# Optimization experiments

Measured on AMD Instinct MI355X. Metric: run time of the kernel, lower is better.

## Reference

```python
import jax, jax.numpy as jnp
import numpy as np

EPS = 1e-5


def gcn_conv(x, W, b, src, dst, ew, num_nodes):
    """GCNConv with add_self_loops=True, symmetric normalization (PyG default)."""
    # degree at destination, self-loop weight 1.0 included implicitly
    deg = jax.ops.segment_sum(ew, dst, num_segments=num_nodes) + 1.0  # [N]
    dinv = jax.lax.rsqrt(deg)                                         # deg >= 1
    norm = dinv[src] * ew * dinv[dst]                                 # [E]
    h = x @ W                                                         # [N, F]
    msg = norm[:, None] * h[src]                                      # [E, F]
    agg = jax.ops.segment_sum(msg, dst, num_segments=num_nodes)       # [N, F]
    # self-loop contribution: dinv[i] * 1 * dinv[i] = 1/deg[i]
    agg = agg + h * (1.0 / deg)[:, None]
    return agg + b


def batchnorm(h, gamma, beta):
    mean = jnp.mean(h, axis=0)
    var = jnp.mean(jnp.square(h - mean), axis=0)  # biased, training-mode stats
    return (h - mean) * jax.lax.rsqrt(var + EPS) * gamma + beta


def setup_inputs() -> dict:
    key = jax.random.key(0)
    ks = jax.random.split(key, 8)
    N, E, F = 50000, 800000, 64
    x = jax.random.normal(ks[0], (N, F), dtype=jnp.float32)
    edge_index = jax.random.randint(ks[1], (2, E), 0, N, dtype=jnp.int64)
    edge_weight = jax.random.uniform(ks[2], (E,), dtype=jnp.float32)
    s = 1.0 / np.sqrt(F)
    W1 = jax.random.uniform(ks[3], (F, F), jnp.float32, -s, s)
    b1 = jnp.zeros((F,), jnp.float32)
    W2 = jax.random.uniform(ks[4], (F, F), jnp.float32, -s, s)
    b2 = jnp.zeros((F,), jnp.float32)
    gamma1 = jnp.ones((F,), jnp.float32)
    beta1 = jnp.zeros((F,), jnp.float32)
    gamma2 = jnp.ones((F,), jnp.float32)
    beta2 = jnp.zeros((F,), jnp.float32)
    return {"x": x, "edge_index": edge_index, "edge_weight": edge_weight,
            "W1": W1, "b1": b1, "gamma1": gamma1, "beta1": beta1,
            "W2": W2, "b2": b2, "gamma2": gamma2, "beta2": beta2}


def reference(x, edge_index, edge_weight, W1, b1, gamma1, beta1, W2, b2, gamma2, beta2):
    N = x.shape[0]
    src, dst = edge_index[0], edge_index[1]
    identity = x
    out = gcn_conv(x, W1, b1, src, dst, edge_weight, N)
    out = jax.nn.relu(batchnorm(out, gamma1, beta1))
    out = gcn_conv(out, W2, b2, src, dst, edge_weight, N)
    out = batchnorm(out, gamma2, beta2)
    out = out + identity  # residual: num_input_features == hidden_dim
    return jax.nn.relu(out)
```

## Files before the change

### kernel.cpp

```cpp
#include <hip/hip_runtime.h>
#include <math.h>

#define FEAT 64
#define BN_EPS 1e-5f
#define BN_REPS 64

__device__ __forceinline__ int edge_idx(const void* p, int is64, long long i) {
    return is64 ? (int)((const long long*)p)[i] : ((const int*)p)[i];
}

__device__ __forceinline__ float4 f4fma(float a, float4 b, float4 c) {
    return make_float4(fmaf(a, b.x, c.x), fmaf(a, b.y, c.y),
                       fmaf(a, b.z, c.z), fmaf(a, b.w, c.w));
}

__device__ __forceinline__ unsigned bf16rtne(float f) {
    unsigned u = __float_as_uint(f);
    return (u + 0x7fffu + ((u >> 16) & 1u)) >> 16;
}
__device__ __forceinline__ unsigned packbf2(float a, float b) {
    return bf16rtne(a) | (bf16rtne(b) << 16);
}
__device__ __forceinline__ float4 unpackbf4(uint2 r) {
    return make_float4(__uint_as_float(r.x << 16),
                       __uint_as_float(r.x & 0xffff0000u),
                       __uint_as_float(r.y << 16),
                       __uint_as_float(r.y & 0xffff0000u));
}

__global__ __launch_bounds__(256) void init_kernel(
    const unsigned* __restrict__ w, int* __restrict__ flag,
    int* __restrict__ cnt, float* __restrict__ parts, int N) {
    int i = blockIdx.x * 256 + threadIdx.x;
    if (i < N) cnt[i] = 0;
    if (blockIdx.x < 64) parts[blockIdx.x * 256 + threadIdx.x] = 0.0f;
    if (blockIdx.x == 0 && threadIdx.x < 64) {
        unsigned long long ok = __ballot(w[2 * threadIdx.x + 1] == 0u);
        if (threadIdx.x == 0) *flag = (ok == ~0ull);
    }
}

__global__ __launch_bounds__(256) void count_seq_kernel(
    const void* __restrict__ ei, const int* __restrict__ flag,
    int* __restrict__ cnt, int* __restrict__ seq, int E) {
    int is64 = *flag;
    int T = gridDim.x * 256;
    int i = blockIdx.x * 256 + threadIdx.x;
#pragma unroll
    for (int u = 0; u < 8; ++u) {
        int e = i + u * T;
        if (e < E) {
            int dst = edge_idx(ei, is64, (long long)E + e);
            seq[e] = atomicAdd(&cnt[dst], 1);
        }
    }
}

__global__ __launch_bounds__(256) void scan1_kernel(const int* __restrict__ cnt,
                                                    int* __restrict__ excl,
                                                    int* __restrict__ bsum, int N) {
    __shared__ int tmp[256];
    int i = blockIdx.x * 256 + threadIdx.x;
    int v = (i < N) ? cnt[i] : 0;
    tmp[threadIdx.x] = v;
    __syncthreads();
    for (int off = 1; off < 256; off <<= 1) {
        int t = (threadIdx.x >= off) ? tmp[threadIdx.x - off] : 0;
        __syncthreads();
        tmp[threadIdx.x] += t;
        __syncthreads();
    }
    if (i < N) excl[i] = tmp[threadIdx.x] - v;
    if (threadIdx.x == 255) bsum[blockIdx.x] = tmp[255];
}

__global__ __launch_bounds__(256) void scan2_kernel(int* __restrict__ bsum, int nb) {
    __shared__ int tmp[256];
    int i = threadIdx.x;
    int v = (i < nb) ? bsum[i] : 0;
    tmp[i] = v;
    __syncthreads();
    for (int off = 1; off < 256; off <<= 1) {
        int t = (i >= off) ? tmp[i - off] : 0;
        __syncthreads();
        tmp[i] += t;
        __syncthreads();
    }
    if (i < nb) bsum[i] = tmp[i] - v;
}

__global__ void scan3_kernel(const int* __restrict__ excl,
                             const int* __restrict__ bsum,
                             int* __restrict__ rowptr, int N, int E) {
    int i = blockIdx.x * 256 + threadIdx.x;
    if (i < N) rowptr[i] = excl[i] + bsum[blockIdx.x];
    if (i == 0) rowptr[N] = E;
}

__global__ __launch_bounds__(256) void scatter_csr_kernel(
    const void* __restrict__ ei, const float* __restrict__ ew,
    const int* __restrict__ flag, const int* __restrict__ rowptr,
    const int* __restrict__ seq, int2* __restrict__ csr, int E) {
    int is64 = *flag;
    int T = gridDim.x * 256;
    int i = blockIdx.x * 256 + threadIdx.x;
#pragma unroll
    for (int u = 0; u < 2; ++u) {
        int e = i + u * T;
        if (e < E) {
            int src = edge_idx(ei, is64, e);
            int dst = edge_idx(ei, is64, (long long)E + e);
            int pos = rowptr[dst] + seq[e];
            csr[pos] = make_int2(src, __float_as_int(ew[e]));
        }
    }
}

__global__ __launch_bounds__(256) void deg_inv_kernel(
    const int* __restrict__ rowptr, const int2* __restrict__ csr,
    float* __restrict__ dinv, float* __restrict__ invdeg, int N) {
    int t = blockIdx.x * 256 + threadIdx.x;
    int n = t >> 3, l = t & 7;
    if (n >= N) return;
    int b = rowptr[n], e = rowptr[n + 1];
    float d = 0.0f;
    for (int k = b + l; k < e; k += 8) d += __int_as_float(csr[k].y);
    d += __shfl_xor(d, 1);
    d += __shfl_xor(d, 2);
    d += __shfl_xor(d, 4);
    if (l == 0) {
        d += 1.0f;
        dinv[n]   = rsqrtf(d);
        invdeg[n] = 1.0f / d;
    }
}

__global__ __launch_bounds__(256) void fold_kernel(int2* __restrict__ csr,
                                                   const float* __restrict__ dinv,
                                                   int E) {
    int T = gridDim.x * 256;
    int i = blockIdx.x * 256 + threadIdx.x;
#pragma unroll
    for (int u = 0; u < 2; ++u) {
        int e = i + u * T;
        if (e < E) {
            int2 v = csr[e];
            csr[e].y = __float_as_int(dinv[v.x] * __int_as_float(v.y));
        }
    }
}

__global__ __launch_bounds__(256) void gemm64_kernel(
    const float* __restrict__ in, const float* __restrict__ W,
    const float* __restrict__ scale, const float* __restrict__ shift,
    uint2* __restrict__ out_bf, int N, int affine) {
    __shared__ float4 Ws4[64][16];
    __shared__ float xs[64][65];
    __shared__ float sA[64], sS[64];
    int tid = threadIdx.x;
    const float4* W4 = (const float4*)W;
    for (int j = tid; j < 1024; j += 256) Ws4[j >> 4][j & 15] = W4[j];
    if (affine && tid < 64) { sA[tid] = scale[tid]; sS[tid] = shift[tid]; }
    __syncthreads();

    int rowBase = blockIdx.x * 64;
    for (int j = tid; j < 1024; j += 256) {
        int r = j >> 4, q = j & 15;
        int row = rowBase + r;
        float4 v = make_float4(0.f, 0.f, 0.f, 0.f);
        if (row < N) {
            v = ((const float4*)in)[(size_t)row * 16 + q];
            if (affine) {
                int c = q * 4;
                v.x = fmaxf(fmaf(v.x, sA[c + 0], sS[c + 0]), 0.f);
                v.y = fmaxf(fmaf(v.y, sA[c + 1], sS[c + 1]), 0.f);
                v.z = fmaxf(fmaf(v.z, sA[c + 2], sS[c + 2]), 0.f);
                v.w = fmaxf(fmaf(v.w, sA[c + 3], sS[c + 3]), 0.f);
            }
        }
        xs[r][q * 4 + 0] = v.x;
        xs[r][q * 4 + 1] = v.y;
        xs[r][q * 4 + 2] = v.z;
        xs[r][q * 4 + 3] = v.w;
    }
    __syncthreads();

    int q = tid & 15, rg = tid >> 4;
    int r0 = rg * 4;
    float4 a0 = make_float4(0.f, 0.f, 0.f, 0.f), a1 = a0, a2 = a0, a3 = a0;
#pragma unroll 4
    for (int k = 0; k < 64; ++k) {
        float4 wv = Ws4[k][q];
        a0 = f4fma(xs[r0 + 0][k], wv, a0);
        a1 = f4fma(xs[r0 + 1][k], wv, a1);
        a2 = f4fma(xs[r0 + 2][k], wv, a2);
        a3 = f4fma(xs[r0 + 3][k], wv, a3);
    }
    int row = rowBase + r0;
    if (row + 0 < N) out_bf[(size_t)(row + 0) * 16 + q] = make_uint2(packbf2(a0.x, a0.y), packbf2(a0.z, a0.w));
    if (row + 1 < N) out_bf[(size_t)(row + 1) * 16 + q] = make_uint2(packbf2(a1.x, a1.y), packbf2(a1.z, a1.w));
    if (row + 2 < N) out_bf[(size_t)(row + 2) * 16 + q] = make_uint2(packbf2(a2.x, a2.y), packbf2(a2.z, a2.w));
    if (row + 3 < N) out_bf[(size_t)(row + 3) * 16 + q] = make_uint2(packbf2(a3.x, a3.y), packbf2(a3.z, a3.w));
}

__global__ __launch_bounds__(256) void gather_agg_kernel(
    const uint2* __restrict__ h2, const int* __restrict__ rowptr,
    const int2* __restrict__ csr, const float* __restrict__ dinv,
    const float* __restrict__ invdeg, const float* __restrict__ bias,
    float* __restrict__ agg, float* __restrict__ parts, int N) {
    int tid = threadIdx.x;
    int wave = tid >> 6, lane = tid & 63;
    int sub = lane >> 4, sl = lane & 15;
    float4 bv = ((const float4*)bias)[sl];
    float4 bnS = make_float4(0.f, 0.f, 0.f, 0.f), bnQ = bnS;

    int n = blockIdx.x * 4 + wave;
    if (n < N) {
        int beg = rowptr[n], end = rowptr[n + 1];
        uint2 selfr = h2[(size_t)n * 16 + sl];
        float dn = dinv[n], idg = invdeg[n];

        float4 accE = make_float4(0.f, 0.f, 0.f, 0.f);
        for (int k = beg; k < end; k += 32) {
            int srcs[8]; float w[8];
#pragma unroll
            for (int j = 0; j < 8; ++j) {
                int idx = k + sub + 4 * j;
                if (idx < end) {
                    unsigned long long v = __builtin_nontemporal_load(
                        (const unsigned long long*)&csr[idx]);
                    srcs[j] = (int)(v & 0xffffffffull);
                    w[j] = __uint_as_float((unsigned)(v >> 32));
                } else { srcs[j] = 0; w[j] = 0.f; }
            }
            uint2 hr[8];
#pragma unroll
            for (int j = 0; j < 8; ++j)
                hr[j] = (k + sub + 4 * j < end)
                          ? h2[(size_t)srcs[j] * 16 + sl] : make_uint2(0u, 0u);
#pragma unroll
            for (int j = 0; j < 8; ++j)
                accE = f4fma(w[j], unpackbf4(hr[j]), accE);
        }
        accE.x += __shfl_xor(accE.x, 16); accE.y += __shfl_xor(accE.y, 16);
        accE.z += __shfl_xor(accE.z, 16); accE.w += __shfl_xor(accE.w, 16);
        accE.x += __shfl_xor(accE.x, 32); accE.y += __shfl_xor(accE.y, 32);
        accE.z += __shfl_xor(accE.z, 32); accE.w += __shfl_xor(accE.w, 32);

        if (sub == 0) {
            float4 self = unpackbf4(selfr);
            float4 tot = f4fma(idg, self, bv);
            tot = f4fma(dn, accE, tot);
            ((float4*)agg)[(size_t)n * 16 + sl] = tot;
            bnS.x += tot.x; bnS.y += tot.y; bnS.z += tot.z; bnS.w += tot.w;
            bnQ.x = fmaf(tot.x, tot.x, bnQ.x); bnQ.y = fmaf(tot.y, tot.y, bnQ.y);
            bnQ.z = fmaf(tot.z, tot.z, bnQ.z); bnQ.w = fmaf(tot.w, tot.w, bnQ.w);
        }
    }

    __shared__ float4 LS[4][16], LQ[4][16];
    if (sub == 0) { LS[wave][sl] = bnS; LQ[wave][sl] = bnQ; }
    __syncthreads();
    if (tid < 16) {
        float4 ts = LS[0][tid], tq = LQ[0][tid];
        for (int i = 1; i < 4; ++i) {
            float4 a = LS[i][tid], b = LQ[i][tid];
            ts.x += a.x; ts.y += a.y; ts.z += a.z; ts.w += a.w;
            tq.x += b.x; tq.y += b.y; tq.z += b.z; tq.w += b.w;
        }
        float* P = parts + (size_t)(blockIdx.x & (BN_REPS - 1)) * 128;
        int c = tid * 4;
        unsafeAtomicAdd(&P[c + 0], ts.x);      unsafeAtomicAdd(&P[c + 1], ts.y);
        unsafeAtomicAdd(&P[c + 2], ts.z);      unsafeAtomicAdd(&P[c + 3], ts.w);
        unsafeAtomicAdd(&P[64 + c + 0], tq.x); unsafeAtomicAdd(&P[64 + c + 1], tq.y);
        unsafeAtomicAdd(&P[64 + c + 2], tq.z); unsafeAtomicAdd(&P[64 + c + 3], tq.w);
    }
}

__global__ void bn_final_kernel(const float* __restrict__ parts,
                                const float* __restrict__ gamma,
                                const float* __restrict__ beta,
                                float* __restrict__ a, float* __restrict__ s,
                                float invN) {
    int c = threadIdx.x;
    if (c < 64) {
        float sm = 0.f, sq = 0.f;
        for (int r = 0; r < BN_REPS; ++r) {
            sm += parts[r * 128 + c];
            sq += parts[r * 128 + 64 + c];
        }
        float m = sm * invN;
        float var = fmaxf(sq * invN - m * m, 0.0f);
        float aa = gamma[c] * rsqrtf(var + BN_EPS);
        a[c] = aa;
        s[c] = beta[c] - m * aa;
    }
}

__global__ void final_out_kernel(const float* __restrict__ agg,
                                 const float* __restrict__ a,
                                 const float* __restrict__ s,
                                 const float* __restrict__ x,
                                 float* __restrict__ out, int nquads) {
    int gid = blockIdx.x * 256 + threadIdx.x;
    if (gid < nquads) {
        int q = gid & 15;
        float4 av = ((const float4*)a)[q], sv = ((const float4*)s)[q];
        float4 g = ((const float4*)agg)[gid], xv = ((const float4*)x)[gid];
        float4 o;
        o.x = fmaxf(fmaf(g.x, av.x, sv.x) + xv.x, 0.f);
        o.y = fmaxf(fmaf(g.y, av.y, sv.y) + xv.y, 0.f);
        o.z = fmaxf(fmaf(g.z, av.z, sv.z) + xv.z, 0.f);
        o.w = fmaxf(fmaf(g.w, av.w, sv.w) + xv.w, 0.f);
        ((float4*)out)[gid] = o;
    }
}

extern "C" void kernel_launch(void* const* d_in, const int* in_sizes, int n_in,
                              void* d_out, int out_size, void* d_ws, size_t ws_size,
                              hipStream_t stream) {
    const float* x      = (const float*)d_in[0];
    const void*  ei     = d_in[1];
    const float* ew     = (const float*)d_in[2];
    const float* W1     = (const float*)d_in[3];
    const float* b1     = (const float*)d_in[4];
    const float* gamma1 = (const float*)d_in[5];
    const float* beta1  = (const float*)d_in[6];
    const float* W2     = (const float*)d_in[7];
    const float* b2     = (const float*)d_in[8];
    const float* gamma2 = (const float*)d_in[9];
    const float* beta2  = (const float*)d_in[10];
    float* out = (float*)d_out;

    const int N = in_sizes[0] / FEAT;
    const int E = in_sizes[2];

    char* ws = (char*)d_ws;
    size_t off = 0;
    auto alloc = [&](size_t bytes) {
        size_t o = off;
        off += (bytes + 255) & ~(size_t)255;
        return (void*)(ws + o);
    };
    int*   flag   = (int*)  alloc(256);
    int*   cnt    = (int*)  alloc((size_t)N * 4);
    int*   rowptr = (int*)  alloc((size_t)(N + 1) * 4);
    int*   seq    = (int*)  alloc((size_t)E * 4);
    int*   excl   = (int*)  alloc((size_t)N * 4);
    int*   bsum   = (int*)  alloc(256 * 4);
    float* dinv   = (float*)alloc((size_t)N * 4);
    float* invdeg = (float*)alloc((size_t)N * 4);
    float* parts  = (float*)alloc(2 * BN_REPS * 128 * 4);
    float* ab     = (float*)alloc(256 * 4);
    int2*  csr    = (int2*) alloc((size_t)E * 8);
    uint2* h_bf   = (uint2*)alloc((size_t)N * 16 * 8);
    float* agg    = (float*)alloc((size_t)N * FEAT * 4);

    const int nblkN  = (N + 255) / 256;
    const int nblkN8 = (N * 8 + 255) / 256;
    const int nblkE8 = (E + 2047) / 2048;
    const int nblkE2 = (E + 511) / 512;
    const int nblkQ  = (N * 16 + 255) / 256;
    const int nblkG  = (N + 63) / 64;
    const int nblkA  = (N + 3) / 4;

    init_kernel<<<nblkN, 256, 0, stream>>>((const unsigned*)ei, flag, cnt, parts, N);
    count_seq_kernel<<<nblkE8, 256, 0, stream>>>(ei, flag, cnt, seq, E);
    scan1_kernel<<<nblkN, 256, 0, stream>>>(cnt, excl, bsum, N);
    scan2_kernel<<<1, 256, 0, stream>>>(bsum, nblkN);
    scan3_kernel<<<nblkN, 256, 0, stream>>>(excl, bsum, rowptr, N, E);
    scatter_csr_kernel<<<nblkE2, 256, 0, stream>>>(ei, ew, flag, rowptr, seq, csr, E);
    deg_inv_kernel<<<nblkN8, 256, 0, stream>>>(rowptr, csr, dinv, invdeg, N);
    fold_kernel<<<nblkE2, 256, 0, stream>>>(csr, dinv, E);

    gemm64_kernel<<<nblkG, 256, 0, stream>>>(x, W1, nullptr, nullptr, h_bf, N, 0);
    gather_agg_kernel<<<nblkA, 256, 0, stream>>>(h_bf, rowptr, csr, dinv,
                                                 invdeg, b1, agg, parts, N);
    bn_final_kernel<<<1, 64, 0, stream>>>(parts, gamma1, beta1,
                                          ab, ab + 64, 1.0f / (float)N);

    gemm64_kernel<<<nblkG, 256, 0, stream>>>(agg, W2, ab, ab + 64, h_bf, N, 1);
    gather_agg_kernel<<<nblkA, 256, 0, stream>>>(h_bf, rowptr, csr, dinv,
                                                 invdeg, b2, agg,
                                                 parts + BN_REPS * 128, N);
    bn_final_kernel<<<1, 64, 0, stream>>>(parts + BN_REPS * 128, gamma2, beta2,
                                          ab + 128, ab + 192, 1.0f / (float)N);

    final_out_kernel<<<nblkQ, 256, 0, stream>>>(agg, ab + 128, ab + 192, x,
                                                out, N * 16);
}
```

Before: 209.0 us.

## Fuse BN finalize into consumers and co-launch edge counting with first GEMM

Removes the two single-block bn_final launches by having every block of the second GEMM and of the output kernel recompute BN scale and shift from the partial sums. The first GEMM shares a grid with the edge-count kernel, so the two independent jobs run in one launch. BN_REPS drops from 64 to 16, which makes the redundant per-block reduction cheaper but raises atomic contention on the partial-sum slots. The intent is fewer launches and less serialization.

```diff
diff --git a/kernel.cpp b/kernel.cpp
--- a/kernel.cpp
+++ b/kernel.cpp
@@ -3,7 +3,7 @@
 
 #define FEAT 64
 #define BN_EPS 1e-5f
-#define BN_REPS 64
+#define BN_REPS 16
 
 __device__ __forceinline__ int edge_idx(const void* p, int is64, long long i) {
     return is64 ? (int)((const long long*)p)[i] : ((const int*)p)[i];
@@ -33,27 +33,71 @@
     int* __restrict__ cnt, float* __restrict__ parts, int N) {
     int i = blockIdx.x * 256 + threadIdx.x;
     if (i < N) cnt[i] = 0;
-    if (blockIdx.x < 64) parts[blockIdx.x * 256 + threadIdx.x] = 0.0f;
+    if (blockIdx.x < 16) parts[blockIdx.x * 256 + threadIdx.x] = 0.0f;
     if (blockIdx.x == 0 && threadIdx.x < 64) {
         unsigned long long ok = __ballot(w[2 * threadIdx.x + 1] == 0u);
         if (threadIdx.x == 0) *flag = (ok == ~0ull);
     }
 }
 
-__global__ __launch_bounds__(256) void count_seq_kernel(
+__global__ __launch_bounds__(256) void fused_count_gemm1_kernel(
     const void* __restrict__ ei, const int* __restrict__ flag,
-    int* __restrict__ cnt, int* __restrict__ seq, int E) {
-    int is64 = *flag;
-    int T = gridDim.x * 256;
-    int i = blockIdx.x * 256 + threadIdx.x;
-#pragma unroll
-    for (int u = 0; u < 8; ++u) {
-        int e = i + u * T;
-        if (e < E) {
-            int dst = edge_idx(ei, is64, (long long)E + e);
-            seq[e] = atomicAdd(&cnt[dst], 1);
-        }
-    }
+    int* __restrict__ cnt, int* __restrict__ seq, int E,
+    const float* __restrict__ x, const float* __restrict__ W1,
+    uint2* __restrict__ out_bf, int N, int nc) {
+    __shared__ float4 Ws4[64][16];
+    __shared__ float xs[64][65];
+    int tid = threadIdx.x;
+
+    if ((int)blockIdx.x < nc) {
+        int is64 = *flag;
+        int T = nc * 256;
+        int i = blockIdx.x * 256 + tid;
+#pragma unroll
+        for (int u = 0; u < 8; ++u) {
+            int e = i + u * T;
+            if (e < E) {
+                int dst = edge_idx(ei, is64, (long long)E + e);
+                seq[e] = atomicAdd(&cnt[dst], 1);
+            }
+        }
+        return;
+    }
+
+    int gb = blockIdx.x - nc;
+    const float4* W4 = (const float4*)W1;
+    for (int j = tid; j < 1024; j += 256) Ws4[j >> 4][j & 15] = W4[j];
+    __syncthreads();
+
+    int rowBase = gb * 64;
+    for (int j = tid; j < 1024; j += 256) {
+        int r = j >> 4, q = j & 15;
+        int row = rowBase + r;
+        float4 v = make_float4(0.f, 0.f, 0.f, 0.f);
+        if (row < N) v = ((const float4*)x)[(size_t)row * 16 + q];
+        xs[r][q * 4 + 0] = v.x;
+        xs[r][q * 4 + 1] = v.y;
+        xs[r][q * 4 + 2] = v.z;
+        xs[r][q * 4 + 3] = v.w;
+    }
+    __syncthreads();
+
+    int q = tid & 15, rg = tid >> 4;
+    int r0 = rg * 4;
+    float4 a0 = make_float4(0.f, 0.f, 0.f, 0.f), a1 = a0, a2 = a0, a3 = a0;
+#pragma unroll 4
+    for (int k = 0; k < 64; ++k) {
+        float4 wv = Ws4[k][q];
+        a0 = f4fma(xs[r0 + 0][k], wv, a0);
+        a1 = f4fma(xs[r0 + 1][k], wv, a1);
+        a2 = f4fma(xs[r0 + 2][k], wv, a2);
+        a3 = f4fma(xs[r0 + 3][k], wv, a3);
+    }
+    int row = rowBase + r0;
+    if (row + 0 < N) out_bf[(size_t)(row + 0) * 16 + q] = make_uint2(packbf2(a0.x, a0.y), packbf2(a0.z, a0.w));
+    if (row + 1 < N) out_bf[(size_t)(row + 1) * 16 + q] = make_uint2(packbf2(a1.x, a1.y), packbf2(a1.z, a1.w));
+    if (row + 2 < N) out_bf[(size_t)(row + 2) * 16 + q] = make_uint2(packbf2(a2.x, a2.y), packbf2(a2.z, a2.w));
+    if (row + 3 < N) out_bf[(size_t)(row + 3) * 16 + q] = make_uint2(packbf2(a3.x, a3.y), packbf2(a3.z, a3.w));
 }
 
 __global__ __launch_bounds__(256) void scan1_kernel(const int* __restrict__ cnt,
@@ -150,17 +194,30 @@
     }
 }
 
-__global__ __launch_bounds__(256) void gemm64_kernel(
+__global__ __launch_bounds__(256) void gemm2_kernel(
     const float* __restrict__ in, const float* __restrict__ W,
-    const float* __restrict__ scale, const float* __restrict__ shift,
-    uint2* __restrict__ out_bf, int N, int affine) {
+    const float* __restrict__ parts, const float* __restrict__ gamma,
+    const float* __restrict__ beta, uint2* __restrict__ out_bf,
+    int N, float invN) {
     __shared__ float4 Ws4[64][16];
     __shared__ float xs[64][65];
     __shared__ float sA[64], sS[64];
     int tid = threadIdx.x;
     const float4* W4 = (const float4*)W;
     for (int j = tid; j < 1024; j += 256) Ws4[j >> 4][j & 15] = W4[j];
-    if (affine && tid < 64) { sA[tid] = scale[tid]; sS[tid] = shift[tid]; }
+    if (tid < 64) {
+        float sm = 0.f, sq = 0.f;
+#pragma unroll
+        for (int r = 0; r < BN_REPS; ++r) {
+            sm += parts[r * 128 + tid];
+            sq += parts[r * 128 + 64 + tid];
+        }
+        float m = sm * invN;
+        float var = fmaxf(sq * invN - m * m, 0.0f);
+        float aa = gamma[tid] * rsqrtf(var + BN_EPS);
+        sA[tid] = aa;
+        sS[tid] = beta[tid] - m * aa;
+    }
     __syncthreads();
 
     int rowBase = blockIdx.x * 64;
@@ -170,13 +227,11 @@
         float4 v = make_float4(0.f, 0.f, 0.f, 0.f);
         if (row < N) {
             v = ((const float4*)in)[(size_t)row * 16 + q];
-            if (affine) {
-                int c = q * 4;
-                v.x = fmaxf(fmaf(v.x, sA[c + 0], sS[c + 0]), 0.f);
-                v.y = fmaxf(fmaf(v.y, sA[c + 1], sS[c + 1]), 0.f);
-                v.z = fmaxf(fmaf(v.z, sA[c + 2], sS[c + 2]), 0.f);
-                v.w = fmaxf(fmaf(v.w, sA[c + 3], sS[c + 3]), 0.f);
-            }
+            int c = q * 4;
+            v.x = fmaxf(fmaf(v.x, sA[c + 0], sS[c + 0]), 0.f);
+            v.y = fmaxf(fmaf(v.y, sA[c + 1], sS[c + 1]), 0.f);
+            v.z = fmaxf(fmaf(v.z, sA[c + 2], sS[c + 2]), 0.f);
+            v.w = fmaxf(fmaf(v.w, sA[c + 3], sS[c + 3]), 0.f);
         }
         xs[r][q * 4 + 0] = v.x;
         xs[r][q * 4 + 1] = v.y;
@@ -277,41 +332,36 @@
     }
 }
 
-__global__ void bn_final_kernel(const float* __restrict__ parts,
-                                const float* __restrict__ gamma,
-                                const float* __restrict__ beta,
-                                float* __restrict__ a, float* __restrict__ s,
-                                float invN) {
-    int c = threadIdx.x;
-    if (c < 64) {
+__global__ __launch_bounds__(256) void final_out_kernel(
+    const float* __restrict__ agg, const float* __restrict__ parts,
+    const float* __restrict__ gamma, const float* __restrict__ beta,
+    const float* __restrict__ x, float* __restrict__ out,
+    int nquads, float invN) {
+    __shared__ float sA[64], sS[64];
+    int tid = threadIdx.x;
+    if (tid < 64) {
         float sm = 0.f, sq = 0.f;
+#pragma unroll
         for (int r = 0; r < BN_REPS; ++r) {
-            sm += parts[r * 128 + c];
-            sq += parts[r * 128 + 64 + c];
+            sm += parts[r * 128 + tid];
+            sq += parts[r * 128 + 64 + tid];
         }
         float m = sm * invN;
         float var = fmaxf(sq * invN - m * m, 0.0f);
-        float aa = gamma[c] * rsqrtf(var + BN_EPS);
-        a[c] = aa;
-        s[c] = beta[c] - m * aa;
-    }
-}
-
-__global__ void final_out_kernel(const float* __restrict__ agg,
-                                 const float* __restrict__ a,
-                                 const float* __restrict__ s,
-                                 const float* __restrict__ x,
-                                 float* __restrict__ out, int nquads) {
-    int gid = blockIdx.x * 256 + threadIdx.x;
+        float aa = gamma[tid] * rsqrtf(var + BN_EPS);
+        sA[tid] = aa;
+        sS[tid] = beta[tid] - m * aa;
+    }
+    __syncthreads();
+    int gid = blockIdx.x * 256 + tid;
     if (gid < nquads) {
-        int q = gid & 15;
-        float4 av = ((const float4*)a)[q], sv = ((const float4*)s)[q];
+        int c = (gid & 15) * 4;
         float4 g = ((const float4*)agg)[gid], xv = ((const float4*)x)[gid];
         float4 o;
-        o.x = fmaxf(fmaf(g.x, av.x, sv.x) + xv.x, 0.f);
-        o.y = fmaxf(fmaf(g.y, av.y, sv.y) + xv.y, 0.f);
-        o.z = fmaxf(fmaf(g.z, av.z, sv.z) + xv.z, 0.f);
-        o.w = fmaxf(fmaf(g.w, av.w, sv.w) + xv.w, 0.f);
+        o.x = fmaxf(fmaf(g.x, sA[c + 0], sS[c + 0]) + xv.x, 0.f);
+        o.y = fmaxf(fmaf(g.y, sA[c + 1], sS[c + 1]) + xv.y, 0.f);
+        o.z = fmaxf(fmaf(g.z, sA[c + 2], sS[c + 2]) + xv.z, 0.f);
+        o.w = fmaxf(fmaf(g.w, sA[c + 3], sS[c + 3]) + xv.w, 0.f);
         ((float4*)out)[gid] = o;
     }
 }
@@ -351,41 +401,36 @@
     float* dinv   = (float*)alloc((size_t)N * 4);
     float* invdeg = (float*)alloc((size_t)N * 4);
     float* parts  = (float*)alloc(2 * BN_REPS * 128 * 4);
-    float* ab     = (float*)alloc(256 * 4);
     int2*  csr    = (int2*) alloc((size_t)E * 8);
     uint2* h_bf   = (uint2*)alloc((size_t)N * 16 * 8);
     float* agg    = (float*)alloc((size_t)N * FEAT * 4);
 
     const int nblkN  = (N + 255) / 256;
-    const int nblkN8 = (N * 8 + 255) / 256;
-    const int nblkE8 = (E + 2047) / 2048;
     const int nblkE2 = (E + 511) / 512;
     const int nblkQ  = (N * 16 + 255) / 256;
     const int nblkG  = (N + 63) / 64;
     const int nblkA  = (N + 3) / 4;
+    const int nc     = (E + 2047) / 2048;
+    const float invN = 1.0f / (float)N;
 
     init_kernel<<<nblkN, 256, 0, stream>>>((const unsigned*)ei, flag, cnt, parts, N);
-    count_seq_kernel<<<nblkE8, 256, 0, stream>>>(ei, flag, cnt, seq, E);
+    fused_count_gemm1_kernel<<<nc + nblkG, 256, 0, stream>>>(
+        ei, flag, cnt, seq, E, x, W1, h_bf, N, nc);
     scan1_kernel<<<nblkN, 256, 0, stream>>>(cnt, excl, bsum, N);
     scan2_kernel<<<1, 256, 0, stream>>>(bsum, nblkN);
     scan3_kernel<<<nblkN, 256, 0, stream>>>(excl, bsum, rowptr, N, E);
     scatter_csr_kernel<<<nblkE2, 256, 0, stream>>>(ei, ew, flag, rowptr, seq, csr, E);
-    deg_inv_kernel<<<nblkN8, 256, 0, stream>>>(rowptr, csr, dinv, invdeg, N);
+    deg_inv_kernel<<<(N * 8 + 255) / 256, 256, 0, stream>>>(rowptr, csr, dinv, invdeg, N);
     fold_kernel<<<nblkE2, 256, 0, stream>>>(csr, dinv, E);
 
-    gemm64_kernel<<<nblkG, 256, 0, stream>>>(x, W1, nullptr, nullptr, h_bf, N, 0);
     gather_agg_kernel<<<nblkA, 256, 0, stream>>>(h_bf, rowptr, csr, dinv,
                                                  invdeg, b1, agg, parts, N);
-    bn_final_kernel<<<1, 64, 0, stream>>>(parts, gamma1, beta1,
-                                          ab, ab + 64, 1.0f / (float)N);
-
-    gemm64_kernel<<<nblkG, 256, 0, stream>>>(agg, W2, ab, ab + 64, h_bf, N, 1);
+    gemm2_kernel<<<nblkG, 256, 0, stream>>>(agg, W2, parts, gamma1, beta1,
+                                            h_bf, N, invN);
     gather_agg_kernel<<<nblkA, 256, 0, stream>>>(h_bf, rowptr, csr, dinv,
                                                  invdeg, b2, agg,
                                                  parts + BN_REPS * 128, N);
-    bn_final_kernel<<<1, 64, 0, stream>>>(parts + BN_REPS * 128, gamma2, beta2,
-                                          ab + 128, ab + 192, 1.0f / (float)N);
-
-    final_out_kernel<<<nblkQ, 256, 0, stream>>>(agg, ab + 128, ab + 192, x,
-                                                out, N * 16);
-}
+    final_out_kernel<<<nblkQ, 256, 0, stream>>>(agg, parts + BN_REPS * 128,
+                                                gamma2, beta2, x, out,
+                                                N * 16, invN);
+}
```

Result: slower. 322.8 us (+54.5%).
